# Kernel tuning notes

Measured on AMD Instinct MI355X. Metric: run time of the kernel, lower is better.

Reference implementation:

```python
import jax, jax.numpy as jnp
import numpy as np

T, B, M, K, N = 8, 1, 16384, 128, 1024


def setup_inputs() -> dict:
    key = jax.random.key(0)
    k1, k2, k3 = jax.random.split(key, 3)
    inputs = jax.random.normal(k1, (T, B, M, K), dtype=jnp.float32)
    weights = jax.random.normal(k2, (T, B, K, N), dtype=jnp.float32) * (1.0 / np.sqrt(K))
    biases = jax.random.normal(k3, (T, 1, 1, N), dtype=jnp.float32)
    return {"inputs": inputs, "weights": weights, "biases": biases}


def reference(inputs, weights, biases):
    # FusedCombineBmm.forward with 3D per-group inputs:
    #   stack -> bmm over T*B -> view [T,B,M,N] -> + stacked bias -> gelu
    # inputs: [T,B,M,K], weights: [T,B,K,N], biases: [T,1,1,N]
    out = jnp.einsum('tbmk,tbkn->tbmn', inputs, weights)
    out = out + biases  # broadcast per-expert bias over (B, M)
    # act == 'gelu' (exact erf form, matching torch's default gelu)
    return jax.nn.gelu(out, approximate=False)
```

## Files before the change

kernel.cpp:

```cpp
#include <hip/hip_runtime.h>

#define T_DIM 8
#define M_DIM 16384
#define K_DIM 128
#define N_DIM 1024

typedef __attribute__((ext_vector_type(8))) short bf16x8_t;
typedef __attribute__((ext_vector_type(4))) float f32x4_t;

__device__ __forceinline__ unsigned short f2bf(float f) {
  unsigned int v;
  __builtin_memcpy(&v, &f, 4);
  v += 0x7FFFu + ((v >> 16) & 1u);
  return (unsigned short)(v >> 16);
}

__device__ __forceinline__ float gelu_tanh(float x) {
  float xc = fminf(fmaxf(x, -8.f), 8.f);
  float y = 2.3022144f * __builtin_fmaf(0.044715f * xc * xc, xc, xc);
  float t = __builtin_amdgcn_exp2f(y);
  return x * t * __builtin_amdgcn_rcpf(t + 1.0f);
}

__global__ __launch_bounds__(256) void transpose_w(
    const float* __restrict__ W, unsigned short* __restrict__ WT) {
  __shared__ __align__(16) unsigned short tile[64][72];
  int b = blockIdx.x;
  int t = b >> 5;
  int r = b & 31;
  int kt = r >> 4;
  int nt = r & 15;
  int tid = threadIdx.x;
  const float* src =
      W + (size_t)t * (K_DIM * N_DIM) + (size_t)(kt * 64) * N_DIM + nt * 64;
#pragma unroll
  for (int it = 0; it < 4; ++it) {
    int li = it * 256 + tid;
    int k = li >> 4;
    int c = li & 15;
    float4 v = *(const float4*)(src + (size_t)k * N_DIM + c * 4);
    unsigned short u[4] = {f2bf(v.x), f2bf(v.y), f2bf(v.z), f2bf(v.w)};
    *(uint2*)&tile[k][c * 4] = *(const uint2*)u;
  }
  __syncthreads();
  unsigned short* dst =
      WT + (size_t)t * (N_DIM * K_DIM) + (size_t)(nt * 64) * K_DIM + kt * 64;
#pragma unroll
  for (int it = 0; it < 2; ++it) {
    int li = it * 256 + tid;
    int n = li >> 3;
    int ck = li & 7;
    __align__(16) unsigned short tmp[8];
#pragma unroll
    for (int j = 0; j < 8; ++j) tmp[j] = tile[ck * 8 + j][n];
    *(uint4*)(dst + (size_t)n * K_DIM + ck * 8) = *(const uint4*)tmp;
  }
}

__global__ __launch_bounds__(256, 2) void gemm_bias_gelu(
    const float* __restrict__ A,
    const unsigned short* __restrict__ WT,
    const float* __restrict__ bias,
    float* __restrict__ O) {
  constexpr int BM = 128, BN = 128, BK = 64;
  constexpr int LDT = 72;
  __shared__ __align__(16) unsigned short smem[2 * 128 * LDT];
  unsigned short* sA = smem;
  unsigned short* sB = smem + 128 * LDT;

  int bid = blockIdx.x;
  int t = bid >> 10;
  int mt = (bid >> 3) & 127;
  int nt = bid & 7;

  int tid = threadIdx.x;
  int lane = tid & 63;
  int wave = tid >> 6;
  int wm = wave & 1;
  int wn = wave >> 1;
  int qk = lane >> 4;
  int lr = lane & 15;

  const float* Ag =
      A + (size_t)t * ((size_t)M_DIM * K_DIM) + (size_t)(mt * BM) * K_DIM;
  const unsigned short* Bg =
      WT + (size_t)t * (N_DIM * K_DIM) + (size_t)(nt * BN) * K_DIM;

  f32x4_t acc[4][4];
#pragma unroll
  for (int i = 0; i < 4; ++i)
#pragma unroll
    for (int j = 0; j < 4; ++j) acc[i][j] = (f32x4_t){0.f, 0.f, 0.f, 0.f};

#pragma unroll
  for (int ks = 0; ks < 2; ++ks) {
    if (ks) __syncthreads();
#pragma unroll
    for (int it = 0; it < 8; ++it) {
      int li = it * 256 + tid;
      int row = li >> 4;
      int c = li & 15;
      float4 va = *(const float4*)(Ag + (size_t)row * K_DIM + ks * BK + c * 4);
      unsigned short u[4] = {f2bf(va.x), f2bf(va.y), f2bf(va.z), f2bf(va.w)};
      *(uint2*)&sA[row * LDT + c * 4] = *(const uint2*)u;
    }
#pragma unroll
    for (int it = 0; it < 4; ++it) {
      int li = it * 256 + tid;
      int row = li >> 3;
      int c = li & 7;
      uint4 vb = *(const uint4*)(Bg + (size_t)row * K_DIM + ks * BK + c * 8);
      *(uint4*)&sB[row * LDT + c * 8] = vb;
    }
    __syncthreads();
#pragma unroll
    for (int kk = 0; kk < 2; ++kk) {
      bf16x8_t af[4], bfv[4];
#pragma unroll
      for (int i = 0; i < 4; ++i) {
        int am = wm * 64 + i * 16 + lr;
        af[i] = *(const bf16x8_t*)&sA[am * LDT + kk * 32 + qk * 8];
        int bn = wn * 64 + i * 16 + lr;
        bfv[i] = *(const bf16x8_t*)&sB[bn * LDT + kk * 32 + qk * 8];
      }
#pragma unroll
      for (int i = 0; i < 4; ++i)
#pragma unroll
        for (int j = 0; j < 4; ++j)
          acc[i][j] = __builtin_amdgcn_mfma_f32_16x16x32_bf16(af[i], bfv[j],
                                                              acc[i][j], 0, 0, 0);
    }
  }

  float bv[4];
#pragma unroll
  for (int j = 0; j < 4; ++j)
    bv[j] = bias[t * N_DIM + nt * BN + wn * 64 + j * 16 + lr];

  float* Og = O + (size_t)t * ((size_t)M_DIM * N_DIM) +
              (size_t)(mt * BM) * N_DIM + nt * BN;
#pragma unroll
  for (int i = 0; i < 4; ++i) {
#pragma unroll
    for (int j = 0; j < 4; ++j) {
#pragma unroll
      for (int rr = 0; rr < 4; ++rr) {
        float x = acc[i][j][rr] + bv[j];
        float g = gelu_tanh(x);
        int m = wm * 64 + i * 16 + qk * 4 + rr;
        int n = wn * 64 + j * 16 + lr;
        Og[(size_t)m * N_DIM + n] = g;
      }
    }
  }
}

extern "C" void kernel_launch(void* const* d_in, const int* in_sizes, int n_in,
                              void* d_out, int out_size, void* d_ws, size_t ws_size,
                              hipStream_t stream) {
  const float* A = (const float*)d_in[0];
  const float* W = (const float*)d_in[1];
  const float* bias = (const float*)d_in[2];
  float* O = (float*)d_out;
  unsigned short* WT = (unsigned short*)d_ws;

  transpose_w<<<256, 256, 0, stream>>>(W, WT);
  gemm_bias_gelu<<<8192, 256, 0, stream>>>(A, WT, bias, O);
}
```

Measured before the change: 671.9 us.

## Keep A row-block resident in LDS and sweep all N tiles with register-loaded B

Each block now converts and stages a 64x128 slice of A once in shared memory, then loops over all eight 128-wide N chunks. B fragments come straight from global memory into registers, with no B staging. This removes the redundant A reloads and fp32-to-bf16 conversions that happened once per N tile. The MFMA operands are swapped so each lane holds four consecutive N values, which allows vectorized nontemporal float4 output stores and a vector bias load. The cost is B reads from global/L2 per block without LDS sharing, plus fewer blocks (2048), each doing a longer serial N loop.

```diff
diff --git a/kernel.cpp b/kernel.cpp
--- a/kernel.cpp
+++ b/kernel.cpp
@@ -57,99 +57,85 @@
   }
 }
 
-__global__ __launch_bounds__(256, 2) void gemm_bias_gelu(
+__global__ __launch_bounds__(256, 3) void gemm_bias_gelu(
     const float* __restrict__ A,
     const unsigned short* __restrict__ WT,
     const float* __restrict__ bias,
     float* __restrict__ O) {
-  constexpr int BM = 128, BN = 128, BK = 64;
-  constexpr int LDT = 72;
-  __shared__ __align__(16) unsigned short smem[2 * 128 * LDT];
-  unsigned short* sA = smem;
-  unsigned short* sB = smem + 128 * LDT;
+  constexpr int BM = 64;
+  constexpr int LDT = 136;
+  __shared__ __align__(16) unsigned short sA[BM * LDT];
 
   int bid = blockIdx.x;
-  int t = bid >> 10;
-  int mt = (bid >> 3) & 127;
-  int nt = bid & 7;
-
+  int t = bid >> 8;
+  int mt = bid & 255;
   int tid = threadIdx.x;
   int lane = tid & 63;
-  int wave = tid >> 6;
-  int wm = wave & 1;
-  int wn = wave >> 1;
+  int wn = tid >> 6;
   int qk = lane >> 4;
   int lr = lane & 15;
 
   const float* Ag =
       A + (size_t)t * ((size_t)M_DIM * K_DIM) + (size_t)(mt * BM) * K_DIM;
-  const unsigned short* Bg =
-      WT + (size_t)t * (N_DIM * K_DIM) + (size_t)(nt * BN) * K_DIM;
+#pragma unroll
+  for (int it = 0; it < 8; ++it) {
+    int li = it * 256 + tid;
+    int row = li >> 5;
+    int c = li & 31;
+    float4 va = *(const float4*)(Ag + (size_t)row * K_DIM + c * 4);
+    unsigned short u[4] = {f2bf(va.x), f2bf(va.y), f2bf(va.z), f2bf(va.w)};
+    *(uint2*)&sA[row * LDT + c * 4] = *(const uint2*)u;
+  }
+  __syncthreads();
 
-  f32x4_t acc[4][4];
+  const unsigned short* Bg = WT + (size_t)t * (N_DIM * K_DIM);
+  const float* bg = bias + t * N_DIM;
+  float* Og = O + (size_t)t * ((size_t)M_DIM * N_DIM) +
+              (size_t)(mt * BM) * N_DIM;
+
+#pragma unroll 1
+  for (int nb = 0; nb < 8; ++nb) {
+    int n0 = nb * 128 + wn * 32;
+
+    bf16x8_t bf[2][4];
 #pragma unroll
-  for (int i = 0; i < 4; ++i)
+    for (int j = 0; j < 2; ++j)
 #pragma unroll
-    for (int j = 0; j < 4; ++j) acc[i][j] = (f32x4_t){0.f, 0.f, 0.f, 0.f};
+      for (int kk = 0; kk < 4; ++kk)
+        bf[j][kk] = *(const bf16x8_t*)(Bg + (size_t)(n0 + j * 16 + lr) * K_DIM +
+                                       kk * 32 + qk * 8);
+
+    f32x4_t acc[4][2];
+#pragma unroll
+    for (int i = 0; i < 4; ++i)
+#pragma unroll
+      for (int j = 0; j < 2; ++j) acc[i][j] = (f32x4_t){0.f, 0.f, 0.f, 0.f};
 
 #pragma unroll
-  for (int ks = 0; ks < 2; ++ks) {
-    if (ks) __syncthreads();
+    for (int kk = 0; kk < 4; ++kk) {
+      bf16x8_t af[4];
 #pragma unroll
-    for (int it = 0; it < 8; ++it) {
-      int li = it * 256 + tid;
-      int row = li >> 4;
-      int c = li & 15;
-      float4 va = *(const float4*)(Ag + (size_t)row * K_DIM + ks * BK + c * 4);
-      unsigned short u[4] = {f2bf(va.x), f2bf(va.y), f2bf(va.z), f2bf(va.w)};
-      *(uint2*)&sA[row * LDT + c * 4] = *(const uint2*)u;
-    }
-#pragma unroll
-    for (int it = 0; it < 4; ++it) {
-      int li = it * 256 + tid;
-      int row = li >> 3;
-      int c = li & 7;
-      uint4 vb = *(const uint4*)(Bg + (size_t)row * K_DIM + ks * BK + c * 8);
-      *(uint4*)&sB[row * LDT + c * 8] = vb;
-    }
-    __syncthreads();
-#pragma unroll
-    for (int kk = 0; kk < 2; ++kk) {
-      bf16x8_t af[4], bfv[4];
-#pragma unroll
-      for (int i = 0; i < 4; ++i) {
-        int am = wm * 64 + i * 16 + lr;
-        af[i] = *(const bf16x8_t*)&sA[am * LDT + kk * 32 + qk * 8];
-        int bn = wn * 64 + i * 16 + lr;
-        bfv[i] = *(const bf16x8_t*)&sB[bn * LDT + kk * 32 + qk * 8];
-      }
+      for (int i = 0; i < 4; ++i)
+        af[i] = *(const bf16x8_t*)&sA[(i * 16 + lr) * LDT + kk * 32 + qk * 8];
 #pragma unroll
       for (int i = 0; i < 4; ++i)
 #pragma unroll
-        for (int j = 0; j < 4; ++j)
-          acc[i][j] = __builtin_amdgcn_mfma_f32_16x16x32_bf16(af[i], bfv[j],
+        for (int j = 0; j < 2; ++j)
+          acc[i][j] = __builtin_amdgcn_mfma_f32_16x16x32_bf16(bf[j][kk], af[i],
                                                               acc[i][j], 0, 0, 0);
     }
-  }
 
-  float bv[4];
 #pragma unroll
-  for (int j = 0; j < 4; ++j)
-    bv[j] = bias[t * N_DIM + nt * BN + wn * 64 + j * 16 + lr];
-
-  float* Og = O + (size_t)t * ((size_t)M_DIM * N_DIM) +
-              (size_t)(mt * BM) * N_DIM + nt * BN;
+    for (int j = 0; j < 2; ++j) {
+      f32x4_t bv = *(const f32x4_t*)(bg + n0 + j * 16 + qk * 4);
 #pragma unroll
-  for (int i = 0; i < 4; ++i) {
+      for (int i = 0; i < 4; ++i) {
+        f32x4_t o;
 #pragma unroll
-    for (int j = 0; j < 4; ++j) {
-#pragma unroll
-      for (int rr = 0; rr < 4; ++rr) {
-        float x = acc[i][j][rr] + bv[j];
-        float g = gelu_tanh(x);
-        int m = wm * 64 + i * 16 + qk * 4 + rr;
-        int n = wn * 64 + j * 16 + lr;
-        Og[(size_t)m * N_DIM + n] = g;
+        for (int rr = 0; rr < 4; ++rr) o[rr] = gelu_tanh(acc[i][j][rr] + bv[rr]);
+        __builtin_nontemporal_store(
+            o, (f32x4_t*)(Og + (size_t)(i * 16 + lr) * N_DIM + n0 + j * 16 +
+                          qk * 4));
       }
     }
   }
@@ -165,5 +151,5 @@
   unsigned short* WT = (unsigned short*)d_ws;
 
   transpose_w<<<256, 256, 0, stream>>>(W, WT);
-  gemm_bias_gelu<<<8192, 256, 0, stream>>>(A, WT, bias, O);
+  gemm_bias_gelu<<<2048, 256, 0, stream>>>(A, WT, bias, O);
 }
```

After: 658.5 us. 2.0% less time.
